# Kernel tuning notes

Measured on AMD Instinct MI355X. Metric: run time of the kernel, lower is better.

## Reference

```python
import jax, jax.numpy as jnp
import numpy as np

B, M, N, I, O, NM = 32, 128, 128, 64, 64, 16


def setup_inputs() -> dict:
    key = jax.random.key(0)
    ks = jax.random.split(key, 10)
    def p(k, shape, s=0.02):
        return jax.random.normal(k, shape, jnp.float32) * s
    g = 1.0 / (I * O)  # xavier_normal_ gain=1/(in*out) -> tiny weights
    return {
        "x": jax.random.normal(ks[0], (B, M, N, I), jnp.float32),
        "w_spec0": p(ks[1], (2, I, O, NM, 2), g),
        "w_spec1": p(ks[2], (2, I, O, NM, 2), g),
        "w_lin": p(ks[3], (I, O)), "b_lin": jnp.zeros((O,), jnp.float32),
        "w_b1": p(ks[4], (O, 2 * O)), "b_b1": jnp.zeros((2 * O,), jnp.float32),
        "w_b2": p(ks[5], (2 * O, O)), "b_b2": jnp.zeros((O,), jnp.float32),
        "w_f1": p(ks[6], (O, 2 * O)), "b_f1": jnp.zeros((2 * O,), jnp.float32),
        "w_f2": p(ks[7], (2 * O, O)), "b_f2": jnp.zeros((O,), jnp.float32),
    }


def _complex_matmul_2d(a, w):
    # a: complex [B, I, x, y]; w: real [2, I, O, NM, 2] (factorized x-weight, y-weight)
    w0 = w[0][..., 0] + 1j * w[0][..., 1]  # [I, O, NM] complex, applied along x
    w1 = w[1][..., 0] + 1j * w[1][..., 1]  # [I, O, NM] complex, applied along y
    c = jnp.einsum('iox,bixy->boxy', w0, a)
    return jnp.einsum('bixy,ioy->boxy', c, w1)


def reference(x, w_spec0, w_spec1, w_lin, b_lin, w_b1, b_b1, w_b2, b_b2,
              w_f1, b_f1, w_f2, b_f2):
    Bv, Mv, Nv, Iv = x.shape
    nm = w_spec0.shape[3]
    Ov = w_spec0.shape[2]
    # residual branch (conv_norm=False -> Identity norm)
    res = x @ w_lin + b_lin  # [B, M, N, O]
    # spectral branch
    xt = jnp.transpose(x, (0, 3, 1, 2))  # [B, I, M, N]
    x_ft = jnp.fft.rfft2(xt, s=(Mv, Nv), norm='ortho')  # [B, I, M, N//2+1] complex64
    out_ft = jnp.zeros((Bv, Ov, Nv, Mv // 2 + 1), dtype=x_ft.dtype)  # M==N in this config
    out_ft = out_ft.at[:, :, :nm, :nm].set(_complex_matmul_2d(x_ft[:, :, :nm, :nm], w_spec0))
    out_ft = out_ft.at[:, :, -nm:, :nm].set(_complex_matmul_2d(x_ft[:, :, -nm:, :nm], w_spec1))
    y = jnp.fft.irfft2(out_ft, s=(Nv, Mv), norm='ortho')  # [B, O, N, M]
    y = jnp.transpose(y, (0, 2, 3, 1))  # [B, M, N, O]
    y = jax.nn.relu(y + res)
    bcast = jax.nn.relu(y @ w_b1 + b_b1) @ w_b2 + b_b2
    fcast = jax.nn.relu(y @ w_f1 + b_f1) @ w_f2 + b_f2
    return (bcast, fcast)
```

## Files before the change

kernel.cpp:

```cpp
#include <hip/hip_runtime.h>
#include <hip/hip_bf16.h>

#define TWO_PI 6.28318530717958647692f

typedef __attribute__((ext_vector_type(8))) short bf16x8;
typedef __attribute__((ext_vector_type(4))) float f32x4;

__device__ __forceinline__ unsigned short f2bf(float v) {
    __hip_bfloat16 h = __float2bfloat16(v);
    return *(unsigned short*)&h;
}

__device__ __forceinline__ bf16x8 cvt8(float4 a, float4 b) {
    bf16x8 r;
    r[0] = (short)f2bf(a.x); r[1] = (short)f2bf(a.y);
    r[2] = (short)f2bf(a.z); r[3] = (short)f2bf(a.w);
    r[4] = (short)f2bf(b.x); r[5] = (short)f2bf(b.y);
    r[6] = (short)f2bf(b.z); r[7] = (short)f2bf(b.w);
    return r;
}

#define SWZ128(row, ch) ((((ch) & 8) | (((ch) ^ ((row) & 7)) & 7)) << 3)


__global__ __launch_bounds__(256) void k0_prep(const float* __restrict__ ws0,
                                               const float* __restrict__ ws1,
                                               unsigned short* __restrict__ w0cc,
                                               unsigned short* __restrict__ w1cc)
{
    int tgt = blockIdx.x * 256 + threadIdx.x;
    int which = tgt >> 19;
    int u = tgt & 524287;
    int ps = u >> 14;
    int plane = (u >> 13) & 1;
    int row = (u >> 7) & 63;
    int k = u & 127;
    int half = k >> 6, e = k & 63;
    float re, im;
    if (which == 0) {
        const float* s = (ps < 16) ? ws0 : ws1;
        int base = ((e * 64 + row) * 16 + (ps & 15)) * 2;
        re = s[base]; im = s[base + 1];
    } else {
        const float* s = ((ps >> 4) ? ws1 : ws0) + 131072;
        int base = ((e * 64 + row) * 16 + (ps & 15)) * 2;
        re = s[base]; im = s[base + 1];
    }
    float val = plane ? (half ? re : im) : (half ? -im : re);
    int ch = k >> 3;
    int dst = ps * 16384 + plane * 8192 + row * 128 + SWZ128(row, ch) + (k & 7);
    (which ? w1cc : w0cc)[dst] = f2bf(val);
}

__global__ __launch_bounds__(256) void k0b_prep(const float* __restrict__ wb1,
                                                const float* __restrict__ wf1,
                                                const float* __restrict__ wb2,
                                                const float* __restrict__ wf2,
                                                const float* __restrict__ wl,
                                                unsigned short* __restrict__ w1bt,
                                                unsigned short* __restrict__ w2bt,
                                                unsigned short* __restrict__ wlt_pre,
                                                unsigned short* __restrict__ ctb_pre,
                                                unsigned short* __restrict__ wdft,
                                                unsigned short* __restrict__ e2k2,
                                                unsigned short* __restrict__ e2k4)
{
    int tgt = blockIdx.x * 256 + threadIdx.x;
    if (tgt < 16384) {
        int head = tgt >> 13;
        int o = (tgt >> 6) & 127;
        int i = tgt & 63;
        const float* src = head ? wf1 : wb1;
        int dst = head * 8192 + o * 64 + (((i >> 3) ^ (o & 7)) << 3) + (i & 7);
        w1bt[dst] = f2bf(src[i * 128 + o]);
    } else if (tgt < 32768) {
        int u = tgt - 16384;
        int head = u >> 13;
        int o = (u >> 7) & 63;
        int c = u & 127;
        const float* src = head ? wf2 : wb2;
        int dst = head * 8192 + o * 128 + (((c >> 3) ^ (o & 7)) << 3) + (c & 7);
        w2bt[dst] = f2bf(src[c * 64 + o]);
    } else if (tgt < 36864) {
        int u = tgt - 32768;
        int o = u >> 6, i = u & 63;
        int chunk = (i >> 3) ^ (o & 7);
        wlt_pre[o * 64 + chunk * 8 + (i & 7)] = f2bf(wl[i * 64 + o]);
    } else if (tgt < 40960) {
        int u = tgt - 36864;
        int v = u >> 5, k = u & 31;
        float val;
        if (k < 16) {
            val = (k == 0) ? (1.0f / 128.0f)
                           : (2.0f / 128.0f) * cosf(TWO_PI * k * v * (1.0f / 128.0f));
        } else {
            int q = k - 16;
            val = (q == 0) ? 0.f
                           : -(2.0f / 128.0f) * sinf(TWO_PI * q * v * (1.0f / 128.0f));
        }
        int chunk = (k >> 3) ^ ((v >> 1) & 3);
        ctb_pre[v * 32 + chunk * 8 + (k & 7)] = f2bf(val);
    } else if (tgt < 45312) {
        int u = tgt - 40960;
        int c = u / 2176;
        int rem = u - c * 2176;
        int kv = rem / 136, n = rem - (rem / 136) * 136;
        float val = 0.f;
        if (n < 128) {
            int idx = (kv * n) & 127;
            float th = (float)idx * (TWO_PI / 128.0f);
            val = c ? -sinf(th) : cosf(th);
        }
        wdft[u] = f2bf(val);
    } else if (tgt < 61696) {
        int u = tgt - 45312;
        int plane = u >> 13;
        int rem = u & 8191;
        int p = rem >> 8;
        int k = rem & 255;
        int km = (p < 16) ? p : (96 + p);
        int m = (k < 128) ? k : (k - 128);
        float th = (float)((km * m) & 127) * (TWO_PI / 128.0f);
        float c = cosf(th), s = sinf(th);
        float val = plane ? ((k < 128) ? -s : c) : ((k < 128) ? c : s);
        val *= (1.0f / 128.0f);
        int ch = k >> 3;
        int dst = plane * 8192 + p * 256 + (((ch & 24) | ((ch ^ p) & 7)) << 3) + (k & 7);
        e2k2[dst] = f2bf(val);
    } else {
        int u = tgt - 61696;
        int plane = u >> 13;
        int rem = u & 8191;
        int uu = rem >> 6;
        int k = rem & 63;
        int p = (k < 32) ? k : (k - 32);
        int km = (p < 16) ? p : (96 + p);
        float th = (float)((km * uu) & 127) * (TWO_PI / 128.0f);
        float c = cosf(th), s = sinf(th);
        float val = plane ? ((k < 32) ? s : c) : ((k < 32) ? c : -s);
        int ch = k >> 3;
        int dst = plane * 8192 + uu * 64 + (((ch ^ (uu & 7)) & 7) << 3) + (k & 7);
        e2k4[dst] = f2bf(val);
    }
}

__global__ __launch_bounds__(256) void k1_dft_n(const float* __restrict__ x,
                                                const unsigned short* __restrict__ wdft,
                                                unsigned int* __restrict__ A)
{
    __shared__ __align__(16) unsigned short Xt[64 * 136];
    __shared__ __align__(16) unsigned short Wl[2 * 16 * 136];
    const int t = threadIdx.x;
    const int bm = blockIdx.x;
    {
        const uint4* wg = (const uint4*)wdft;
        uint4* wl = (uint4*)Wl;
        for (int k = t; k < 544; k += 256) wl[k] = wg[k];
    }
    {
        const float* xg = x + (size_t)bm * 8192;
        const int i = t & 63, q = t >> 6;
        #pragma unroll
        for (int pass = 0; pass < 8; ++pass) {
            int n0 = pass * 16 + q * 4;
            float v0 = xg[(n0 + 0) * 64 + i];
            float v1 = xg[(n0 + 1) * 64 + i];
            float v2 = xg[(n0 + 2) * 64 + i];
            float v3 = xg[(n0 + 3) * 64 + i];
            unsigned lo = (unsigned)f2bf(v0) | ((unsigned)f2bf(v1) << 16);
            unsigned hi = (unsigned)f2bf(v2) | ((unsigned)f2bf(v3) << 16);
            *(uint2*)&Xt[i * 136 + n0] = make_uint2(lo, hi);
        }
    }
    __syncthreads();
    const int lane = t & 63, wv = t >> 6;
    const int ar = lane & 15, kg = lane >> 4;
    f32x4 are = (f32x4){0.f, 0.f, 0.f, 0.f};
    f32x4 aim = (f32x4){0.f, 0.f, 0.f, 0.f};
    #pragma unroll
    for (int ks = 0; ks < 4; ++ks) {
        int off = ks * 32 + kg * 8;
        bf16x8 b   = *(const bf16x8*)&Xt[(wv * 16 + ar) * 136 + off];
        bf16x8 wre = *(const bf16x8*)&Wl[ar * 136 + off];
        bf16x8 wim = *(const bf16x8*)&Wl[(16 + ar) * 136 + off];
        are = __builtin_amdgcn_mfma_f32_16x16x32_bf16(wre, b, are, 0, 0, 0);
        aim = __builtin_amdgcn_mfma_f32_16x16x32_bf16(wim, b, aim, 0, 0, 0);
    }
    unsigned int* Ap = A + (size_t)bm * 1024;
    #pragma unroll
    for (int r = 0; r < 4; ++r) {
        int kv = kg * 4 + r;
        int i = wv * 16 + ar;
        Ap[kv * 64 + i] = (unsigned)f2bf(are[r]) | ((unsigned)f2bf(aim[r]) << 16);
    }
}

__global__ __launch_bounds__(256) void k2_dft_m(const unsigned int* __restrict__ A,
                                                const unsigned short* __restrict__ e2k2,
                                                unsigned int* __restrict__ xftp)
{
    __shared__ __align__(16) unsigned short El[16384];
    __shared__ __align__(16) unsigned short Sl[16384];
    const int t = threadIdx.x;
    const int b = blockIdx.x >> 4, kv = blockIdx.x & 15;
    {
        const uint4* eg = (const uint4*)e2k2;
        for (int k = t; k < 2048; k += 256) ((uint4*)El)[k] = eg[k];
    }
    for (int idx = t; idx < 4096; idx += 256) {
        int m2 = idx >> 6, i = idx & 63;
        int m = m2 << 1;
        unsigned a0 = A[((size_t)(b * 128 + m) * 16 + kv) * 64 + i];
        unsigned a1 = A[((size_t)(b * 128 + m + 1) * 16 + kv) * 64 + i];
        unsigned arp = (a0 & 0xffffu) | (a1 << 16);
        unsigned aip = (a0 >> 16) | (a1 & 0xffff0000u);
        int chr = m >> 3;
        *(unsigned*)&Sl[i * 256 + (((chr & 24) | ((chr ^ i) & 7)) << 3) + (m & 7)] = arp;
        int kk = 128 + m;
        int chi = kk >> 3;
        *(unsigned*)&Sl[i * 256 + (((chi & 24) | ((chi ^ i) & 7)) << 3) + (kk & 7)] = aip;
    }
    __syncthreads();
    const int lane = t & 63, wv = t >> 6;
    const int ar = lane & 15, kg = lane >> 4;
    const int pt = wv >> 1;
    const int it0 = (wv & 1) << 1;
    #pragma unroll
    for (int iti = 0; iti < 2; ++iti) {
        int it = it0 + iti;
        int prow = pt * 16 + ar;
        int irow = it * 16 + ar;
        f32x4 accre = (f32x4){0.f, 0.f, 0.f, 0.f};
        f32x4 accim = (f32x4){0.f, 0.f, 0.f, 0.f};
        #pragma unroll
        for (int ks = 0; ks < 8; ++ks) {
            int ch = ks * 4 + kg;
            int aoff = prow * 256 + (((ch & 24) | ((ch ^ prow) & 7)) << 3);
            int boff = irow * 256 + (((ch & 24) | ((ch ^ irow) & 7)) << 3);
            bf16x8 bfrag = *(const bf16x8*)&Sl[boff];
            bf16x8 fre = *(const bf16x8*)&El[aoff];
            bf16x8 fim = *(const bf16x8*)&El[8192 + aoff];
            accre = __builtin_amdgcn_mfma_f32_16x16x32_bf16(fre, bfrag, accre, 0, 0, 0);
            accim = __builtin_amdgcn_mfma_f32_16x16x32_bf16(fim, bfrag, accim, 0, 0, 0);
        }
        #pragma unroll
        for (int r = 0; r < 4; ++r) {
            int p = pt * 16 + kg * 4 + r;
            int i = it * 16 + ar;
            xftp[((size_t)(b * 32 + p) * 16 + kv) * 64 + i] =
                (unsigned)f2bf(accre[r]) | ((unsigned)f2bf(accim[r]) << 16);
        }
    }
}

__global__ __launch_bounds__(256) void k3a_spec1(const unsigned int* __restrict__ xftp,
                                                 const unsigned short* __restrict__ w0cc,
                                                 unsigned int* __restrict__ c1p)
{
    __shared__ __align__(16) unsigned short As[16 * 128];
    __shared__ __align__(16) unsigned short Ws[2 * 64 * 128];
    const int t = threadIdx.x;
    const int b = blockIdx.x >> 5, p = blockIdx.x & 31;
    {
        const uint4* wg = (const uint4*)(w0cc + (size_t)p * 16384);
        for (int k = t; k < 2048; k += 256) ((uint4*)Ws)[k] = wg[k];
    }
    for (int idx = t; idx < 512; idx += 256) {
        int kvv = idx >> 5, i2 = (idx & 31) << 1;
        const unsigned* src = xftp + ((size_t)(b * 32 + p) * 16 + kvv) * 64;
        unsigned a0 = src[i2], a1 = src[i2 + 1];
        unsigned rep = (a0 & 0xffffu) | (a1 << 16);
        unsigned imp = (a0 >> 16) | (a1 & 0xffff0000u);
        int chr = i2 >> 3;
        *(unsigned*)&As[kvv * 128 + SWZ128(kvv, chr) + (i2 & 7)] = rep;
        int kk = 64 + i2;
        int chi = kk >> 3;
        *(unsigned*)&As[kvv * 128 + SWZ128(kvv, chi) + (kk & 7)] = imp;
    }
    __syncthreads();
    const int lane = t & 63, wv = t >> 6;
    const int ar = lane & 15, kg = lane >> 4;
    const int jrow = wv * 16 + ar;
    f32x4 accre = (f32x4){0.f, 0.f, 0.f, 0.f};
    f32x4 accim = (f32x4){0.f, 0.f, 0.f, 0.f};
    #pragma unroll
    for (int ks = 0; ks < 4; ++ks) {
        int ch = ks * 4 + kg;
        bf16x8 af = *(const bf16x8*)&As[ar * 128 + SWZ128(ar, ch)];
        bf16x8 br = *(const bf16x8*)&Ws[jrow * 128 + SWZ128(jrow, ch)];
        bf16x8 bi = *(const bf16x8*)&Ws[8192 + jrow * 128 + SWZ128(jrow, ch)];
        accre = __builtin_amdgcn_mfma_f32_16x16x32_bf16(af, br, accre, 0, 0, 0);
        accim = __builtin_amdgcn_mfma_f32_16x16x32_bf16(af, bi, accim, 0, 0, 0);
    }
    unsigned int* cp = c1p + ((size_t)(b * 32 + p) * 16) * 64;
    #pragma unroll
    for (int r = 0; r < 4; ++r) {
        int kv = kg * 4 + r;
        cp[kv * 64 + wv * 16 + ar] =
            (unsigned)f2bf(accre[r]) | ((unsigned)f2bf(accim[r]) << 16);
    }
}

__global__ __launch_bounds__(256) void k3b_spec2(const unsigned int* __restrict__ c1p,
                                                 const unsigned short* __restrict__ w1cc,
                                                 unsigned int* __restrict__ oftp)
{
    __shared__ __align__(16) unsigned short As[16 * 128];
    __shared__ __align__(16) unsigned short Ws[2 * 64 * 128];
    const int t = threadIdx.x;
    int id = blockIdx.x;
    const int h = id & 1; id >>= 1;
    const int kv = id & 15; const int b = id >> 4;
    {
        const uint4* wg = (const uint4*)(w1cc + (size_t)(h * 16 + kv) * 16384);
        for (int k = t; k < 2048; k += 256) ((uint4*)Ws)[k] = wg[k];
    }
    for (int idx = t; idx < 512; idx += 256) {
        int pp = idx >> 5, j2 = (idx & 31) << 1;
        const unsigned* src = c1p + ((size_t)(b * 32 + h * 16 + pp) * 16 + kv) * 64;
        unsigned a0 = src[j2], a1 = src[j2 + 1];
        unsigned rep = (a0 & 0xffffu) | (a1 << 16);
        unsigned imp = (a0 >> 16) | (a1 & 0xffff0000u);
        int chr = j2 >> 3;
        *(unsigned*)&As[pp * 128 + SWZ128(pp, chr) + (j2 & 7)] = rep;
        int kk = 64 + j2;
        int chi = kk >> 3;
        *(unsigned*)&As[pp * 128 + SWZ128(pp, chi) + (kk & 7)] = imp;
    }
    __syncthreads();
    const int lane = t & 63, wv = t >> 6;
    const int ar = lane & 15, kg = lane >> 4;
    const int orow = wv * 16 + ar;
    f32x4 accre = (f32x4){0.f, 0.f, 0.f, 0.f};
    f32x4 accim = (f32x4){0.f, 0.f, 0.f, 0.f};
    #pragma unroll
    for (int ks = 0; ks < 4; ++ks) {
        int ch = ks * 4 + kg;
        bf16x8 af = *(const bf16x8*)&As[ar * 128 + SWZ128(ar, ch)];
        bf16x8 br = *(const bf16x8*)&Ws[orow * 128 + SWZ128(orow, ch)];
        bf16x8 bi = *(const bf16x8*)&Ws[8192 + orow * 128 + SWZ128(orow, ch)];
        accre = __builtin_amdgcn_mfma_f32_16x16x32_bf16(af, br, accre, 0, 0, 0);
        accim = __builtin_amdgcn_mfma_f32_16x16x32_bf16(af, bi, accim, 0, 0, 0);
    }
    #pragma unroll
    for (int r = 0; r < 4; ++r) {
        int pp = kg * 4 + r;
        oftp[((size_t)(b * 32 + h * 16 + pp) * 16 + kv) * 64 + orow] =
            (unsigned)f2bf(accre[r]) | ((unsigned)f2bf(accim[r]) << 16);
    }
}

__global__ __launch_bounds__(256) void k4_idft_m(const unsigned int* __restrict__ oftp,
                                                 const unsigned short* __restrict__ e2k4,
                                                 unsigned int* __restrict__ T)
{
    __shared__ __align__(16) unsigned short El[16384];
    __shared__ __align__(16) unsigned short Sl[4096];
    const int t = threadIdx.x;
    const int b = blockIdx.x >> 4, q = blockIdx.x & 15;
    {
        const uint4* eg = (const uint4*)e2k4;
        for (int k = t; k < 2048; k += 256) ((uint4*)El)[k] = eg[k];
    }
    for (int idx = t; idx < 1024; idx += 256) {
        int p2 = idx >> 6, o = idx & 63;
        int p = p2 << 1;
        unsigned a0 = oftp[((size_t)(b * 32 + p) * 16 + q) * 64 + o];
        unsigned a1 = oftp[((size_t)(b * 32 + p + 1) * 16 + q) * 64 + o];
        unsigned rep = (a0 & 0xffffu) | (a1 << 16);
        unsigned imp = (a0 >> 16) | (a1 & 0xffff0000u);
        int chr = p >> 3;
        *(unsigned*)&Sl[o * 64 + ((chr ^ (o & 7)) << 3) + (p & 7)] = rep;
        int kk = 32 + p;
        int chi = kk >> 3;
        *(unsigned*)&Sl[o * 64 + ((chi ^ (o & 7)) << 3) + (kk & 7)] = imp;
    }
    __syncthreads();
    const int lane = t & 63, wv = t >> 6;
    const int ar = lane & 15, kg = lane >> 4;
    unsigned int* Tp = T + ((size_t)b * 128) * 1024 + (size_t)q * 64;
    #pragma unroll
    for (int uti = 0; uti < 2; ++uti) {
        int ut = wv * 2 + uti;
        int urow = ut * 16 + ar;
        int aswz = urow & 7;
        #pragma unroll
        for (int ot = 0; ot < 4; ++ot) {
            int orow = ot * 16 + ar;
            f32x4 accre = (f32x4){0.f, 0.f, 0.f, 0.f};
            f32x4 accim = (f32x4){0.f, 0.f, 0.f, 0.f};
            #pragma unroll
            for (int ks = 0; ks < 2; ++ks) {
                int ch = ks * 4 + kg;
                int aoff = urow * 64 + ((ch ^ aswz) << 3);
                int boff = orow * 64 + ((ch ^ (orow & 7)) << 3);
                bf16x8 bfrag = *(const bf16x8*)&Sl[boff];
                bf16x8 fre = *(const bf16x8*)&El[aoff];
                bf16x8 fim = *(const bf16x8*)&El[8192 + aoff];
                accre = __builtin_amdgcn_mfma_f32_16x16x32_bf16(fre, bfrag, accre, 0, 0, 0);
                accim = __builtin_amdgcn_mfma_f32_16x16x32_bf16(fim, bfrag, accim, 0, 0, 0);
            }
            #pragma unroll
            for (int r = 0; r < 4; ++r) {
                int u = ut * 16 + kg * 4 + r;
                int o = ot * 16 + ar;
                Tp[(size_t)u * 1024 + o] =
                    (unsigned)f2bf(accre[r]) | ((unsigned)f2bf(accim[r]) << 16);
            }
        }
    }
}

__global__ __launch_bounds__(256) void k56_fused(
    const float* __restrict__ x, const unsigned int* __restrict__ Tg,
    const float* __restrict__ bl,
    const unsigned short* __restrict__ ctb_pre, const unsigned short* __restrict__ wlt_pre,
    const unsigned short* __restrict__ w1bt, const unsigned short* __restrict__ w2bt,
    const float* __restrict__ bb1, const float* __restrict__ bb2,
    const float* __restrict__ bf1, const float* __restrict__ bf2,
    float* __restrict__ out)
{
    __shared__ __align__(16) unsigned char U[32768];
    __shared__ __align__(16) unsigned short ys[2][8192];
    __shared__ __align__(16) unsigned short hs[8192];

    unsigned short* Ctb = (unsigned short*)U;
    unsigned short* wlt = (unsigned short*)(U + 8192);
    unsigned short* Tpk = (unsigned short*)(U + 16384);
    unsigned short* w1s = (unsigned short*)U;
    unsigned short* w2s = (unsigned short*)(U + 16384);

    const int t = threadIdx.x;
    const int bm0 = blockIdx.x << 1;
    const int lane = t & 63, wv = t >> 6;
    const int ar = lane & 15, kg = lane >> 4;
    const int R0 = wv * 32;

    float4 xr[2][2][4];
    #pragma unroll
    for (int g = 0; g < 2; ++g)
        #pragma unroll
        for (int rt = 0; rt < 2; ++rt) {
            const float* xp = x + (size_t)(bm0 + g) * 8192 + (R0 + rt * 16 + ar) * 64 + kg * 8;
            xr[g][rt][0] = *(const float4*)(xp);
            xr[g][rt][1] = *(const float4*)(xp + 4);
            xr[g][rt][2] = *(const float4*)(xp + 32);
            xr[g][rt][3] = *(const float4*)(xp + 36);
        }

    {
        const uint4* cg = (const uint4*)ctb_pre;
        for (int k = t; k < 512; k += 256) ((uint4*)Ctb)[k] = cg[k];
        const uint4* wg = (const uint4*)wlt_pre;
        for (int k = t; k < 512; k += 256) ((uint4*)wlt)[k] = wg[k];
        for (int idx = t; idx < 2048; idx += 256) {
            int g = idx >> 10, rem = idx & 1023;
            int q = rem >> 6, o = rem & 63;
            unsigned v = Tg[(size_t)(bm0 + g) * 1024 + rem];
            int f = (o >> 1) & 3;
            unsigned short* Tp = Tpk + g * 2048;
            Tp[o * 32 + (((q >> 3) ^ f) << 3) + (q & 7)] = (unsigned short)(v & 0xffffu);
            Tp[o * 32 + (((2 + (q >> 3)) ^ f) << 3) + (q & 7)] = (unsigned short)(v >> 16);
        }
    }
    __syncthreads();

    float biasl[4];
    #pragma unroll
    for (int ct = 0; ct < 4; ++ct) biasl[ct] = bl[ct * 16 + ar];

    #pragma unroll
    for (int g = 0; g < 2; ++g) {
        const unsigned short* Tp = Tpk + g * 2048;
        #pragma unroll
        for (int rt = 0; rt < 2; ++rt) {
            const int vrow = R0 + rt * 16 + ar;
            bf16x8 a0 = cvt8(xr[g][rt][0], xr[g][rt][1]);
            bf16x8 a1 = cvt8(xr[g][rt][2], xr[g][rt][3]);
            bf16x8 asp = *(const bf16x8*)&Ctb[vrow * 32 + ((kg ^ ((vrow >> 1) & 3)) << 3)];
            f32x4 acc[4];
            #pragma unroll
            for (int ct = 0; ct < 4; ++ct) acc[ct] = (f32x4){0.f, 0.f, 0.f, 0.f};
            #pragma unroll
            for (int ct = 0; ct < 4; ++ct) {
                int o = ct * 16 + ar;
                bf16x8 b0 = *(const bf16x8*)&wlt[o * 64 + ((kg ^ (o & 7)) << 3)];
                bf16x8 b1 = *(const bf16x8*)&wlt[o * 64 + (((4 + kg) ^ (o & 7)) << 3)];
                bf16x8 bsp = *(const bf16x8*)&Tp[o * 32 + ((kg ^ ((o >> 1) & 3)) << 3)];
                acc[ct] = __builtin_amdgcn_mfma_f32_16x16x32_bf16(a0, b0, acc[ct], 0, 0, 0);
                acc[ct] = __builtin_amdgcn_mfma_f32_16x16x32_bf16(a1, b1, acc[ct], 0, 0, 0);
                acc[ct] = __builtin_amdgcn_mfma_f32_16x16x32_bf16(asp, bsp, acc[ct], 0, 0, 0);
            }
            #pragma unroll
            for (int ct = 0; ct < 4; ++ct) {
                int col = ct * 16 + ar;
                #pragma unroll
                for (int r = 0; r < 4; ++r) {
                    int row = R0 + rt * 16 + kg * 4 + r;
                    float v = fmaxf(acc[ct][r] + biasl[ct], 0.f);
                    ys[g][row * 64 + (((col >> 3) ^ (row & 7)) << 3) + (col & 7)] = f2bf(v);
                }
            }
        }
    }
    __syncthreads();

    unsigned short* hw = hs + wv * 2048;
    for (int head = 0; head < 2; ++head) {
        {
            const uint4* g1 = (const uint4*)(w1bt + head * 8192);
            for (int k = t; k < 1024; k += 256) ((uint4*)w1s)[k] = g1[k];
            const uint4* g2 = (const uint4*)(w2bt + head * 8192);
            for (int k = t; k < 1024; k += 256) ((uint4*)w2s)[k] = g2[k];
        }
        const float* B1 = head ? bf1 : bb1;
        const float* B2 = head ? bf2 : bb2;
        float bias1[8], bias2[4];
        #pragma unroll
        for (int c = 0; c < 8; ++c) bias1[c] = B1[c * 16 + ar];
        #pragma unroll
        for (int c = 0; c < 4; ++c) bias2[c] = B2[c * 16 + ar];
        __syncthreads();

        #pragma unroll
        for (int g = 0; g < 2; ++g) {
            #pragma unroll
            for (int rt = 0; rt < 2; ++rt) {
                const int rowbase = R0 + rt * 16;
                const int yrow = rowbase + ar;
                bf16x8 ya0 = *(const bf16x8*)&ys[g][yrow * 64 + ((kg ^ (yrow & 7)) << 3)];
                bf16x8 ya1 = *(const bf16x8*)&ys[g][yrow * 64 + (((4 + kg) ^ (yrow & 7)) << 3)];
                f32x4 acc1[8];
                #pragma unroll
                for (int ct = 0; ct < 8; ++ct) acc1[ct] = (f32x4){0.f, 0.f, 0.f, 0.f};
                #pragma unroll
                for (int ct = 0; ct < 8; ++ct) {
                    int brow = ct * 16 + ar;
                    bf16x8 b0 = *(const bf16x8*)&w1s[brow * 64 + ((kg ^ (brow & 7)) << 3)];
                    bf16x8 b1 = *(const bf16x8*)&w1s[brow * 64 + (((4 + kg) ^ (brow & 7)) << 3)];
                    acc1[ct] = __builtin_amdgcn_mfma_f32_16x16x32_bf16(ya0, b0, acc1[ct], 0, 0, 0);
                    acc1[ct] = __builtin_amdgcn_mfma_f32_16x16x32_bf16(ya1, b1, acc1[ct], 0, 0, 0);
                }
                #pragma unroll
                for (int ct = 0; ct < 8; ++ct) {
                    #pragma unroll
                    for (int r = 0; r < 4; ++r) {
                        int row = kg * 4 + r;
                        int col = ct * 16 + ar;
                        float v = fmaxf(acc1[ct][r] + bias1[ct], 0.f);
                        hw[row * 128 + (((col >> 3) ^ (row & 7)) << 3) + (col & 7)] = f2bf(v);
                    }
                }
                f32x4 acc2[4];
                #pragma unroll
                for (int ct = 0; ct < 4; ++ct) acc2[ct] = (f32x4){0.f, 0.f, 0.f, 0.f};
                #pragma unroll
                for (int ks = 0; ks < 4; ++ks) {
                    bf16x8 a = *(const bf16x8*)&hw[ar * 128 + (((ks * 4 + kg) ^ (ar & 7)) << 3)];
                    #pragma unroll
                    for (int ct = 0; ct < 4; ++ct) {
                        int brow = ct * 16 + ar;
                        bf16x8 b = *(const bf16x8*)&w2s[brow * 128 + (((ks * 4 + kg) ^ (ar & 7)) << 3)];
                        acc2[ct] = __builtin_amdgcn_mfma_f32_16x16x32_bf16(a, b, acc2[ct], 0, 0, 0);
                    }
                }
                float* og = out + (size_t)head * 33554432u + (size_t)(bm0 + g) * 8192;
                #pragma unroll
                for (int ct = 0; ct < 4; ++ct) {
                    #pragma unroll
                    for (int r = 0; r < 4; ++r)
                        og[(size_t)(rowbase + kg * 4 + r) * 64 + ct * 16 + ar] =
                            acc2[ct][r] + bias2[ct];
                }
            }
        }
        if (head == 0) __syncthreads();
    }
}

extern "C" void kernel_launch(void* const* d_in, const int* in_sizes, int n_in,
                              void* d_out, int out_size, void* d_ws, size_t ws_size,
                              hipStream_t stream)
{
    (void)in_sizes; (void)n_in; (void)out_size; (void)ws_size;
    const float* x   = (const float*)d_in[0];
    const float* ws0 = (const float*)d_in[1];
    const float* ws1 = (const float*)d_in[2];
    const float* wl  = (const float*)d_in[3];
    const float* bl  = (const float*)d_in[4];
    const float* wb1 = (const float*)d_in[5];
    const float* bb1 = (const float*)d_in[6];
    const float* wb2 = (const float*)d_in[7];
    const float* bb2 = (const float*)d_in[8];
    const float* wf1 = (const float*)d_in[9];
    const float* bf1 = (const float*)d_in[10];
    const float* wf2 = (const float*)d_in[11];
    const float* bf2 = (const float*)d_in[12];
    float* out = (float*)d_out;

    float* ws = (float*)d_ws;
    unsigned short* w0cc = (unsigned short*)ws;
    unsigned short* w1cc = (unsigned short*)(ws + 262144);
    unsigned int* Tb   = (unsigned int*)(ws + 524288);
    unsigned int* Ab   = (unsigned int*)(ws + 8912896);
    unsigned int* xftp = (unsigned int*)(ws + 17301504);
    unsigned int* c1p  = (unsigned int*)(ws + 19398656);
    unsigned int* oftp = (unsigned int*)(ws + 21495808);
    unsigned short* w1bt    = (unsigned short*)(ws + 23592960);
    unsigned short* w2bt    = (unsigned short*)(ws + 23601152);
    unsigned short* wlt_pre = (unsigned short*)(ws + 23609344);
    unsigned short* ctb_pre = (unsigned short*)(ws + 23611392);
    unsigned short* wdft    = (unsigned short*)(ws + 23613440);
    unsigned short* e2k2    = (unsigned short*)(ws + 23615616);
    unsigned short* e2k4    = (unsigned short*)(ws + 23623808);

    k0_prep    <<<4096, 256, 0, stream>>>(ws0, ws1, w0cc, w1cc);
    k0b_prep   <<<305,  256, 0, stream>>>(wb1, wf1, wb2, wf2, wl,
                                          w1bt, w2bt, wlt_pre, ctb_pre, wdft,
                                          e2k2, e2k4);
    k1_dft_n   <<<4096, 256, 0, stream>>>(x, wdft, Ab);
    k2_dft_m   <<<512,  256, 0, stream>>>(Ab, e2k2, xftp);
    k3a_spec1  <<<1024, 256, 0, stream>>>(xftp, w0cc, c1p);
    k3b_spec2  <<<1024, 256, 0, stream>>>(c1p, w1cc, oftp);
    k4_idft_m  <<<512,  256, 0, stream>>>(oftp, e2k4, Tb);
    k56_fused  <<<2048, 256, 0, stream>>>(x, Tb, bl, ctb_pre, wlt_pre,
                                          w1bt, w2bt, bb1, bb2, bf1, bf2, out);
}
```

Before: 192.2 us.

## Split fused assembly/heads kernel into separate assembly and MLP-head kernels

Splits the fused kernel into two. k5_assem computes relu(x@Wlin + spectral + b) per row block and writes bf16 y to a global workspace. k6_heads reads y straight into registers and runs both MLP heads. The goal is lower LDS use and register pressure per kernel, which should raise occupancy. The cost is an extra global write and read of y (about 32 MB of bf16) plus one more launch.

Result: slower. 214.1 us (+11.4%).

```diff
diff --git a/kernel.cpp b/kernel.cpp
--- a/kernel.cpp
+++ b/kernel.cpp
@@ -411,24 +411,99 @@
     }
 }
 
-__global__ __launch_bounds__(256) void k56_fused(
+__global__ __launch_bounds__(256) void k5_assem(
     const float* __restrict__ x, const unsigned int* __restrict__ Tg,
     const float* __restrict__ bl,
     const unsigned short* __restrict__ ctb_pre, const unsigned short* __restrict__ wlt_pre,
+    unsigned short* __restrict__ yg)
+{
+    __shared__ __align__(16) unsigned short Ctb[4096];
+    __shared__ __align__(16) unsigned short wlt[4096];
+    __shared__ __align__(16) unsigned short Tpk[2048];
+    __shared__ __align__(16) unsigned short ys[8192];
+
+    const int t = threadIdx.x;
+    const int bm = blockIdx.x;
+    const int lane = t & 63, wv = t >> 6;
+    const int ar = lane & 15, kg = lane >> 4;
+    const int R0 = wv * 32;
+
+    float4 xr[2][4];
+    #pragma unroll
+    for (int rt = 0; rt < 2; ++rt) {
+        const float* xp = x + (size_t)bm * 8192 + (R0 + rt * 16 + ar) * 64 + kg * 8;
+        xr[rt][0] = *(const float4*)(xp);
+        xr[rt][1] = *(const float4*)(xp + 4);
+        xr[rt][2] = *(const float4*)(xp + 32);
+        xr[rt][3] = *(const float4*)(xp + 36);
+    }
+    {
+        const uint4* cg = (const uint4*)ctb_pre;
+        for (int k = t; k < 512; k += 256) ((uint4*)Ctb)[k] = cg[k];
+        const uint4* wg = (const uint4*)wlt_pre;
+        for (int k = t; k < 512; k += 256) ((uint4*)wlt)[k] = wg[k];
+        const unsigned int* Tp = Tg + (size_t)bm * 1024;
+        for (int idx = t; idx < 1024; idx += 256) {
+            int q = idx >> 6, o = idx & 63;
+            unsigned v = Tp[idx];
+            int f = (o >> 1) & 3;
+            Tpk[o * 32 + (((q >> 3) ^ f) << 3) + (q & 7)] = (unsigned short)(v & 0xffffu);
+            Tpk[o * 32 + (((2 + (q >> 3)) ^ f) << 3) + (q & 7)] = (unsigned short)(v >> 16);
+        }
+    }
+    __syncthreads();
+
+    float biasl[4];
+    #pragma unroll
+    for (int ct = 0; ct < 4; ++ct) biasl[ct] = bl[ct * 16 + ar];
+
+    #pragma unroll
+    for (int rt = 0; rt < 2; ++rt) {
+        const int vrow = R0 + rt * 16 + ar;
+        bf16x8 a0 = cvt8(xr[rt][0], xr[rt][1]);
+        bf16x8 a1 = cvt8(xr[rt][2], xr[rt][3]);
+        bf16x8 asp = *(const bf16x8*)&Ctb[vrow * 32 + ((kg ^ ((vrow >> 1) & 3)) << 3)];
+        f32x4 acc[4];
+        #pragma unroll
+        for (int ct = 0; ct < 4; ++ct) acc[ct] = (f32x4){0.f, 0.f, 0.f, 0.f};
+        #pragma unroll
+        for (int ct = 0; ct < 4; ++ct) {
+            int o = ct * 16 + ar;
+            bf16x8 b0 = *(const bf16x8*)&wlt[o * 64 + ((kg ^ (o & 7)) << 3)];
+            bf16x8 b1 = *(const bf16x8*)&wlt[o * 64 + (((4 + kg) ^ (o & 7)) << 3)];
+            bf16x8 bsp = *(const bf16x8*)&Tpk[o * 32 + ((kg ^ ((o >> 1) & 3)) << 3)];
+            acc[ct] = __builtin_amdgcn_mfma_f32_16x16x32_bf16(a0, b0, acc[ct], 0, 0, 0);
+            acc[ct] = __builtin_amdgcn_mfma_f32_16x16x32_bf16(a1, b1, acc[ct], 0, 0, 0);
+            acc[ct] = __builtin_amdgcn_mfma_f32_16x16x32_bf16(asp, bsp, acc[ct], 0, 0, 0);
+        }
+        #pragma unroll
+        for (int ct = 0; ct < 4; ++ct) {
+            int col = ct * 16 + ar;
+            #pragma unroll
+            for (int r = 0; r < 4; ++r) {
+                int row = R0 + rt * 16 + kg * 4 + r;
+                float v = fmaxf(acc[ct][r] + biasl[ct], 0.f);
+                ys[row * 64 + (((col >> 3) ^ (row & 7)) << 3) + (col & 7)] = f2bf(v);
+            }
+        }
+    }
+    __syncthreads();
+
+    uint4* yo = (uint4*)(yg + (size_t)bm * 8192);
+    const uint4* yi = (const uint4*)ys;
+    for (int k = t; k < 1024; k += 256) yo[k] = yi[k];
+}
+
+__global__ __launch_bounds__(256) void k6_heads(
+    const unsigned short* __restrict__ yg,
     const unsigned short* __restrict__ w1bt, const unsigned short* __restrict__ w2bt,
     const float* __restrict__ bb1, const float* __restrict__ bb2,
     const float* __restrict__ bf1, const float* __restrict__ bf2,
     float* __restrict__ out)
 {
-    __shared__ __align__(16) unsigned char U[32768];
-    __shared__ __align__(16) unsigned short ys[2][8192];
+    __shared__ __align__(16) unsigned short w1s[8192];
+    __shared__ __align__(16) unsigned short w2s[8192];
     __shared__ __align__(16) unsigned short hs[8192];
-
-    unsigned short* Ctb = (unsigned short*)U;
-    unsigned short* wlt = (unsigned short*)(U + 8192);
-    unsigned short* Tpk = (unsigned short*)(U + 16384);
-    unsigned short* w1s = (unsigned short*)U;
-    unsigned short* w2s = (unsigned short*)(U + 16384);
 
     const int t = threadIdx.x;
     const int bm0 = blockIdx.x << 1;
@@ -436,74 +511,16 @@
     const int ar = lane & 15, kg = lane >> 4;
     const int R0 = wv * 32;
 
-    float4 xr[2][2][4];
+    bf16x8 yf[2][2][2];
     #pragma unroll
     for (int g = 0; g < 2; ++g)
         #pragma unroll
         for (int rt = 0; rt < 2; ++rt) {
-            const float* xp = x + (size_t)(bm0 + g) * 8192 + (R0 + rt * 16 + ar) * 64 + kg * 8;
-            xr[g][rt][0] = *(const float4*)(xp);
-            xr[g][rt][1] = *(const float4*)(xp + 4);
-            xr[g][rt][2] = *(const float4*)(xp + 32);
-            xr[g][rt][3] = *(const float4*)(xp + 36);
-        }
-
-    {
-        const uint4* cg = (const uint4*)ctb_pre;
-        for (int k = t; k < 512; k += 256) ((uint4*)Ctb)[k] = cg[k];
-        const uint4* wg = (const uint4*)wlt_pre;
-        for (int k = t; k < 512; k += 256) ((uint4*)wlt)[k] = wg[k];
-        for (int idx = t; idx < 2048; idx += 256) {
-            int g = idx >> 10, rem = idx & 1023;
-            int q = rem >> 6, o = rem & 63;
-            unsigned v = Tg[(size_t)(bm0 + g) * 1024 + rem];
-            int f = (o >> 1) & 3;
-            unsigned short* Tp = Tpk + g * 2048;
-            Tp[o * 32 + (((q >> 3) ^ f) << 3) + (q & 7)] = (unsigned short)(v & 0xffffu);
-            Tp[o * 32 + (((2 + (q >> 3)) ^ f) << 3) + (q & 7)] = (unsigned short)(v >> 16);
-        }
-    }
-    __syncthreads();
-
-    float biasl[4];
-    #pragma unroll
-    for (int ct = 0; ct < 4; ++ct) biasl[ct] = bl[ct * 16 + ar];
-
-    #pragma unroll
-    for (int g = 0; g < 2; ++g) {
-        const unsigned short* Tp = Tpk + g * 2048;
-        #pragma unroll
-        for (int rt = 0; rt < 2; ++rt) {
-            const int vrow = R0 + rt * 16 + ar;
-            bf16x8 a0 = cvt8(xr[g][rt][0], xr[g][rt][1]);
-            bf16x8 a1 = cvt8(xr[g][rt][2], xr[g][rt][3]);
-            bf16x8 asp = *(const bf16x8*)&Ctb[vrow * 32 + ((kg ^ ((vrow >> 1) & 3)) << 3)];
-            f32x4 acc[4];
-            #pragma unroll
-            for (int ct = 0; ct < 4; ++ct) acc[ct] = (f32x4){0.f, 0.f, 0.f, 0.f};
-            #pragma unroll
-            for (int ct = 0; ct < 4; ++ct) {
-                int o = ct * 16 + ar;
-                bf16x8 b0 = *(const bf16x8*)&wlt[o * 64 + ((kg ^ (o & 7)) << 3)];
-                bf16x8 b1 = *(const bf16x8*)&wlt[o * 64 + (((4 + kg) ^ (o & 7)) << 3)];
-                bf16x8 bsp = *(const bf16x8*)&Tp[o * 32 + ((kg ^ ((o >> 1) & 3)) << 3)];
-                acc[ct] = __builtin_amdgcn_mfma_f32_16x16x32_bf16(a0, b0, acc[ct], 0, 0, 0);
-                acc[ct] = __builtin_amdgcn_mfma_f32_16x16x32_bf16(a1, b1, acc[ct], 0, 0, 0);
-                acc[ct] = __builtin_amdgcn_mfma_f32_16x16x32_bf16(asp, bsp, acc[ct], 0, 0, 0);
-            }
-            #pragma unroll
-            for (int ct = 0; ct < 4; ++ct) {
-                int col = ct * 16 + ar;
-                #pragma unroll
-                for (int r = 0; r < 4; ++r) {
-                    int row = R0 + rt * 16 + kg * 4 + r;
-                    float v = fmaxf(acc[ct][r] + biasl[ct], 0.f);
-                    ys[g][row * 64 + (((col >> 3) ^ (row & 7)) << 3) + (col & 7)] = f2bf(v);
-                }
-            }
-        }
-    }
-    __syncthreads();
+            const int yrow = R0 + rt * 16 + ar;
+            const unsigned short* yp = yg + (size_t)(bm0 + g) * 8192 + yrow * 64;
+            yf[g][rt][0] = *(const bf16x8*)&yp[(kg ^ (yrow & 7)) << 3];
+            yf[g][rt][1] = *(const bf16x8*)&yp[((4 + kg) ^ (yrow & 7)) << 3];
+        }
 
     unsigned short* hw = hs + wv * 2048;
     for (int head = 0; head < 2; ++head) {
@@ -527,9 +544,6 @@
             #pragma unroll
             for (int rt = 0; rt < 2; ++rt) {
                 const int rowbase = R0 + rt * 16;
-                const int yrow = rowbase + ar;
-                bf16x8 ya0 = *(const bf16x8*)&ys[g][yrow * 64 + ((kg ^ (yrow & 7)) << 3)];
-                bf16x8 ya1 = *(const bf16x8*)&ys[g][yrow * 64 + (((4 + kg) ^ (yrow & 7)) << 3)];
                 f32x4 acc1[8];
                 #pragma unroll
                 for (int ct = 0; ct < 8; ++ct) acc1[ct] = (f32x4){0.f, 0.f, 0.f, 0.f};
@@ -538,8 +552,8 @@
                     int brow = ct * 16 + ar;
                     bf16x8 b0 = *(const bf16x8*)&w1s[brow * 64 + ((kg ^ (brow & 7)) << 3)];
                     bf16x8 b1 = *(const bf16x8*)&w1s[brow * 64 + (((4 + kg) ^ (brow & 7)) << 3)];
-                    acc1[ct] = __builtin_amdgcn_mfma_f32_16x16x32_bf16(ya0, b0, acc1[ct], 0, 0, 0);
-                    acc1[ct] = __builtin_amdgcn_mfma_f32_16x16x32_bf16(ya1, b1, acc1[ct], 0, 0, 0);
+                    acc1[ct] = __builtin_amdgcn_mfma_f32_16x16x32_bf16(yf[g][rt][0], b0, acc1[ct], 0, 0, 0);
+                    acc1[ct] = __builtin_amdgcn_mfma_f32_16x16x32_bf16(yf[g][rt][1], b1, acc1[ct], 0, 0, 0);
                 }
                 #pragma unroll
                 for (int ct = 0; ct < 8; ++ct) {
@@ -613,6 +627,7 @@
     unsigned short* wdft    = (unsigned short*)(ws + 23613440);
     unsigned short* e2k2    = (unsigned short*)(ws + 23615616);
     unsigned short* e2k4    = (unsigned short*)(ws + 23623808);
+    unsigned short* yg      = (unsigned short*)(ws + 23632000);
 
     k0_prep    <<<4096, 256, 0, stream>>>(ws0, ws1, w0cc, w1cc);
     k0b_prep   <<<305,  256, 0, stream>>>(wb1, wf1, wb2, wf2, wl,
@@ -623,6 +638,6 @@
     k3a_spec1  <<<1024, 256, 0, stream>>>(xftp, w0cc, c1p);
     k3b_spec2  <<<1024, 256, 0, stream>>>(c1p, w1cc, oftp);
     k4_idft_m  <<<512,  256, 0, stream>>>(oftp, e2k4, Tb);
-    k56_fused  <<<2048, 256, 0, stream>>>(x, Tb, bl, ctb_pre, wlt_pre,
-                                          w1bt, w2bt, bb1, bb2, bf1, bf2, out);
-}
+    k5_assem   <<<4096, 256, 0, stream>>>(x, Tb, bl, ctb_pre, wlt_pre, yg);
+    k6_heads   <<<2048, 256, 0, stream>>>(yg, w1bt, w2bt, bb1, bb2, bf1, bf2, out);
+}
```
